# Kernel optimization log

Measured on AMD Instinct MI355X. Metric: run time of the kernel, lower is better.

The kernel has to match this reference:

```python
import jax, jax.numpy as jnp
import numpy as np
from jax import lax

N, T, IN, H, HEADS, OUT, E = 20000, 32, 32, 64, 4, 1, 320000


def setup_inputs() -> dict:
    key = jax.random.key(0)
    ks = jax.random.split(key, 18)
    s = 0.1
    inp = {
        "x": jax.random.normal(ks[0], (N, T, IN), jnp.float32),
        "edge_index": jax.random.randint(ks[1], (2, E), 0, N, dtype=jnp.int32),
        # LSTM layer 0 (PyTorch gate order i,f,g,o)
        "l0_Wih": jax.random.normal(ks[2], (4 * H, IN), jnp.float32) * s,
        "l0_Whh": jax.random.normal(ks[3], (4 * H, H), jnp.float32) * s,
        "l0_bih": jax.random.normal(ks[4], (4 * H,), jnp.float32) * s,
        "l0_bhh": jax.random.normal(ks[5], (4 * H,), jnp.float32) * s,
        # LSTM layer 1
        "l1_Wih": jax.random.normal(ks[6], (4 * H, H), jnp.float32) * s,
        "l1_Whh": jax.random.normal(ks[7], (4 * H, H), jnp.float32) * s,
        "l1_bih": jax.random.normal(ks[8], (4 * H,), jnp.float32) * s,
        "l1_bhh": jax.random.normal(ks[9], (4 * H,), jnp.float32) * s,
        # GAT layer 1: in=H, out=H, heads=HEADS (concat)
        "g1_w": jax.random.normal(ks[10], (H, HEADS * H), jnp.float32) * s,
        "g1_as": jax.random.normal(ks[11], (1, HEADS, H), jnp.float32) * s,
        "g1_ad": jax.random.normal(ks[12], (1, HEADS, H), jnp.float32) * s,
        "g1_b": jnp.zeros((HEADS * H,), jnp.float32),
        # GAT layer 2: in=HEADS*H, out=OUT, heads=1
        "g2_w": jax.random.normal(ks[13], (HEADS * H, OUT), jnp.float32) * s,
        "g2_as": jax.random.normal(ks[14], (1, 1, OUT), jnp.float32) * s,
        "g2_ad": jax.random.normal(ks[15], (1, 1, OUT), jnp.float32) * s,
        "g2_b": jnp.zeros((OUT,), jnp.float32),
    }
    return inp


def _lstm_layer(x, Wih, Whh, bih, bhh):
    # x: [N, T, F] -> [N, T, H]
    n = x.shape[0]
    h0 = jnp.zeros((n, Whh.shape[1]), x.dtype)

    def step(carry, xt):
        h, c = carry
        g = xt @ Wih.T + h @ Whh.T + bih + bhh  # [N, 4H]
        i, f, gg, o = jnp.split(g, 4, axis=-1)
        c = jax.nn.sigmoid(f) * c + jax.nn.sigmoid(i) * jnp.tanh(gg)
        h = jax.nn.sigmoid(o) * jnp.tanh(c)
        return (h, c), h

    _, hs = lax.scan(step, (h0, h0), jnp.swapaxes(x, 0, 1))
    return jnp.swapaxes(hs, 0, 1)


def _gat(x, src, dst, n, W, a_src, a_dst, b, heads, outc):
    # PyG GATConv (eval mode, add_self_loops already applied to src/dst)
    xh = (x @ W).reshape(n, heads, outc)              # [N, heads, C]
    al_s = (xh * a_src).sum(-1)                       # [N, heads]
    al_d = (xh * a_dst).sum(-1)
    e = jax.nn.leaky_relu(al_s[src] + al_d[dst], 0.2)  # [E, heads]
    m = jax.ops.segment_max(e, dst, num_segments=n)
    m = jnp.where(jnp.isfinite(m), m, 0.0)
    ex = jnp.exp(e - m[dst])
    den = jax.ops.segment_sum(ex, dst, num_segments=n)
    w = ex / (den[dst] + 1e-16)                       # segment softmax over dst
    out = jax.ops.segment_sum(xh[src] * w[..., None], dst, num_segments=n)
    return out.reshape(n, heads * outc) + b


def reference(x, edge_index, l0_Wih, l0_Whh, l0_bih, l0_bhh, l1_Wih, l1_Whh,
              l1_bih, l1_bhh, g1_w, g1_as, g1_ad, g1_b, g2_w, g2_as, g2_ad, g2_b):
    n = x.shape[0]
    loops = jnp.arange(n, dtype=edge_index.dtype)
    ei = jnp.concatenate([edge_index, jnp.stack([loops, loops])], axis=1)
    src, dst = ei[0], ei[1]
    h = _lstm_layer(x, l0_Wih, l0_Whh, l0_bih, l0_bhh)
    h = _lstm_layer(h, l1_Wih, l1_Whh, l1_bih, l1_bhh)
    h = h[:, -1, :]  # node features from last timestep
    h = jax.nn.relu(_gat(h, src, dst, n, g1_w, g1_as, g1_ad, g1_b, HEADS, H))
    return _gat(h, src, dst, n, g2_w, g2_as, g2_ad, g2_b, 1, OUT)
```

## Files before the change

### kernel.cpp

```cpp
#include <hip/hip_runtime.h>
#include <math.h>

#define NN   20000
#define TT   32
#define INF_ 32
#define HID  64
#define NH   4
#define EE   320000
#define ETOT (EE + NN)
#define ZROW 168
#define NB   80

typedef __attribute__((ext_vector_type(8))) short bf16x8;
typedef __attribute__((ext_vector_type(4))) float f32x4;

static __device__ __forceinline__ float lrelu(float x){ return x>0.0f ? x : 0.2f*x; }

static __device__ __forceinline__ unsigned short f2bf(float f){
  unsigned u = __float_as_uint(f);
  unsigned r = u + 0x7fffu + ((u>>16)&1u);
  return (unsigned short)(r>>16);
}
static __device__ __forceinline__ float bf2f(unsigned short h){ return __uint_as_float(((unsigned)h)<<16); }

static __device__ __forceinline__ int zpos(int kq){
  return (kq&3) + (((kq>>4)&1)<<2) + (((kq>>2)&3)<<3);
}

static __device__ __forceinline__ float lstm_cell(float gi, float gf, float gg, float go, float& c){
  float ef = __expf(-gf), ei = __expf(-gi), eg = __expf(-2.0f*gg);
  float pN = c*(1.0f+ei)*(1.0f+eg) + (1.0f-eg)*(1.0f+ef);
  float pD = (1.0f+ef)*(1.0f+ei)*(1.0f+eg);
  float cc = pN * __builtin_amdgcn_rcpf(pD);
  c = cc;
  float eo = __expf(-go), ec = __expf(-2.0f*cc);
  return (1.0f-ec) * __builtin_amdgcn_rcpf((1.0f+eo)*(1.0f+ec));
}

static __device__ __forceinline__ void edge_sd(const int* __restrict__ ei, int e, int& s, int& d){
  if (e < EE){ s = ei[e]; d = ei[EE + e]; } else { s = e - EE; d = s; }
}

__global__ void kzero_int(int* __restrict__ p, int n){
  int i = blockIdx.x*256 + threadIdx.x;
  if (i < n) p[i] = 0;
}

__global__ void pack_weights(const float* __restrict__ Wih0, const float* __restrict__ Whh0,
                             const float* __restrict__ bih0, const float* __restrict__ bhh0,
                             const float* __restrict__ Wih1, const float* __restrict__ Whh1,
                             const float* __restrict__ bih1, const float* __restrict__ bhh1,
                             unsigned short* __restrict__ Wpk,
                             float* __restrict__ b0, float* __restrict__ b1){
  int idx = blockIdx.x*256 + threadIdx.x;
  if (idx < 49152){
    int fb = idx >> 9;
    int h  = fb & 1;
    int t2 = fb >> 1;
    int ks = t2 % 3, tl = t2 / 3;
    int r  = idx & 511;
    int l  = r >> 3, j = r & 7;
    int pr = l & 15;
    int g  = (pr&3)*64 + tl*4 + (pr>>2);
    int k  = ks*32 + 4*(l>>4) + (j & 3) + 16*(j >> 2);
    float src = (k < 32) ? Wih0[g*32 + k] : Whh0[g*64 + (k - 32)];
    unsigned short hi = f2bf(src);
    Wpk[idx] = h ? f2bf(src - bf2f(hi)) : hi;
  } else if (idx < 114688){
    int idx2 = idx - 49152;
    int fb = idx2 >> 9;
    int h  = fb & 1;
    int t2 = fb >> 1;
    int ks = t2 & 3, tl = t2 >> 2;
    int r  = idx2 & 511;
    int l  = r >> 3, j = r & 7;
    int pr = l & 15;
    int g  = (pr&3)*64 + tl*4 + (pr>>2);
    int k  = ks*32 + 4*(l>>4) + (j & 3) + 16*(j >> 2);
    float src = (k < 64) ? Wih1[g*64 + k] : Whh1[g*64 + (k - 64)];
    unsigned short hi = f2bf(src);
    Wpk[idx] = h ? f2bf(src - bf2f(hi)) : hi;
  } else {
    int m = idx - 114688;
    if (m < 256) b0[m] = bih0[m] + bhh0[m];
    else if (m < 512) b1[m-256] = bih1[m-256] + bhh1[m-256];
  }
}

__global__ void count_deg(const int* __restrict__ ei, int* __restrict__ deg){
  int e = blockIdx.x*256 + threadIdx.x;
  if (e >= ETOT) return;
  int s, d; edge_sd(ei, e, s, d);
  atomicAdd(deg + d, 1);
}

__global__ void scan_deg(const int* __restrict__ deg, int* __restrict__ indptr, int* __restrict__ cursor){
  __shared__ int part[256];
  const int t = threadIdx.x;
  const int CH = (NN + 255) / 256;
  const int c0 = t * CH;
  int sum = 0;
  for (int i=0;i<CH;i++){ int idx=c0+i; if (idx<NN) sum += deg[idx]; }
  part[t] = sum; __syncthreads();
  int val = sum;
  for (int off=1; off<256; off<<=1){
    int add = (t>=off) ? part[t-off] : 0;
    __syncthreads();
    val += add; part[t] = val;
    __syncthreads();
  }
  int run = val - sum;
  for (int i=0;i<CH;i++){
    int idx=c0+i;
    if (idx<NN){ indptr[idx]=run; cursor[idx]=run; run += deg[idx]; }
  }
  if (t == 0) indptr[NN] = ETOT;
}

__global__ void scatter_edges(const int* __restrict__ ei, int* __restrict__ cursor, int* __restrict__ csr_src){
  int e = blockIdx.x*256 + threadIdx.x;
  if (e >= ETOT) return;
  int s, d; edge_sd(ei, e, s, d);
  int pos = atomicAdd(cursor + d, 1);
  csr_src[pos] = s;
}

#define PIN_LOAD(dst, p) asm volatile( \
    "global_load_dwordx4 %0, %1, off\n\t" \
    "s_waitcnt vmcnt(0)" \
    : "=&v"(dst) : "v"(p))

__global__ __launch_bounds__(1024)
__attribute__((amdgpu_waves_per_eu(4, 4)))
void lstm_mfma(
    const float* __restrict__ x,
    const unsigned short* __restrict__ Wpk,
    const float* __restrict__ b0, const float* __restrict__ b1,
    float* __restrict__ h1out)
{
  __shared__ unsigned short Zh[NB*ZROW];
  __shared__ unsigned short Zl[NB*ZROW];

  const int tid  = threadIdx.x;
  const int lane = tid & 63;
  const int w    = __builtin_amdgcn_readfirstlane(tid >> 6);
  const int ln15 = lane & 15;
  const int lq   = lane >> 4;
  const int gbase = blockIdx.x * NB;

  const bf16x8* wp = (const bf16x8*)Wpk;

  bf16x8 wA0h[3], wA0l[3], wA1h[4], wA1l[4];
#pragma unroll
  for (int ks=0; ks<3; ++ks){
    PIN_LOAD(wA0h[ks], wp + ((w*3+ks)*2+0)*64 + lane);
    PIN_LOAD(wA0l[ks], wp + ((w*3+ks)*2+1)*64 + lane);
  }
#pragma unroll
  for (int ks=0; ks<4; ++ks){
    PIN_LOAD(wA1h[ks], wp + 6144 + ((w*4+ks)*2+0)*64 + lane);
    PIN_LOAD(wA1l[ks], wp + 6144 + ((w*4+ks)*2+1)*64 + lane);
  }

  f32x4 bv0, bv1;
  {
    const int u = w*4 + lq;
#pragma unroll
    for (int j=0; j<4; ++j){ bv0[j] = b0[j*64+u]; bv1[j] = b1[j*64+u]; }
  }

  const int hs_ = lq + ((w & 4) ? 4 : 0) + 8*(w & 3);
  const int uc0 = (1 + (w>>3))*32 + hs_;
  const int uc1 = (3 + (w>>3))*32 + hs_;

  const int xn = tid >> 3;
  const int xk = (tid & 7) * 4;
  const int xslot = (((xk>>2)&3)<<3) + (((xk>>4)&1)<<2);
  const float* xp = x + (size_t)(gbase + ((xn < NB) ? xn : 0))*(TT*INF_) + xk;
  const bool xth = (tid < 640);

#define XSTAGE(v) {                                                       \
    unsigned pkA, pkB, plA, plB;                                          \
    asm("v_cvt_pk_bf16_f32 %0,%1,%2":"=v"(pkA):"v"((v).x),"v"((v).y));    \
    asm("v_cvt_pk_bf16_f32 %0,%1,%2":"=v"(pkB):"v"((v).z),"v"((v).w));    \
    float l0_ = (v).x - __uint_as_float(pkA<<16);                         \
    float l1_ = (v).y - __uint_as_float(pkA & 0xffff0000u);               \
    float l2_ = (v).z - __uint_as_float(pkB<<16);                         \
    float l3_ = (v).w - __uint_as_float(pkB & 0xffff0000u);               \
    asm("v_cvt_pk_bf16_f32 %0,%1,%2":"=v"(plA):"v"(l0_),"v"(l1_));        \
    asm("v_cvt_pk_bf16_f32 %0,%1,%2":"=v"(plB):"v"(l2_),"v"(l3_));        \
    *(uint2*)&Zh[xn*ZROW + xslot] = make_uint2(pkA, pkB);                 \
    *(uint2*)&Zl[xn*ZROW + xslot] = make_uint2(plA, plB); }

  for (int i = tid; i < NB*ZROW/2; i += 1024){ ((unsigned*)Zh)[i] = 0; ((unsigned*)Zl)[i] = 0; }
  __syncthreads();
  if (xth){
    float4 v = *(const float4*)xp;
    XSTAGE(v);
  }
  __syncthreads();

  float c0[5], c1[5];
#pragma unroll
  for (int i=0;i<5;i++){ c0[i]=0.f; c1[i]=0.f; }
  f32x4 aL1[5];

#define ZFRAG(Zb, node, ck) (*(const bf16x8*)&Zb[(node)*ZROW + (ck)*32 + lq*8])

#define MF(acc, A, B) acc = __builtin_amdgcn_mfma_f32_16x16x32_bf16((A),(B),(acc),0,0,0)

#define WPAIR(ha, hb, GA, GB, col) {                                      \
    unsigned pk_, pl_;                                                    \
    asm("v_cvt_pk_bf16_f32 %0,%1,%2":"=v"(pk_):"v"(ha),"v"(hb));          \
    float la_ = (ha) - __uint_as_float(pk_<<16);                          \
    float lb_ = (hb) - __uint_as_float(pk_ & 0xffff0000u);                \
    asm("v_cvt_pk_bf16_f32 %0,%1,%2":"=v"(pl_):"v"(la_),"v"(lb_));        \
    Zh[((GA)*16+ln15)*ZROW + (col)] = (unsigned short)pk_;                \
    Zh[((GB)*16+ln15)*ZROW + (col)] = (unsigned short)(pk_>>16);          \
    Zl[((GA)*16+ln15)*ZROW + (col)] = (unsigned short)pl_;                \
    Zl[((GB)*16+ln15)*ZROW + (col)] = (unsigned short)(pl_>>16); }

#define WSINGLE(hv, GG, col) {                                            \
    const int _n = (GG)*16 + ln15;                                        \
    const unsigned short _hh = f2bf(hv);                                  \
    Zh[_n*ZROW + (col)] = _hh;                                            \
    Zl[_n*ZROW + (col)] = f2bf((hv) - bf2f(_hh)); }

#define CHUNK(ACCS, CK, WH, WL)                                           \
    _Pragma("unroll")                                                     \
    for (int GG=0; GG<5; ++GG){                                           \
      const bf16x8 zh = ZFRAG(Zh, GG*16+ln15, CK);                        \
      const bf16x8 zl = ZFRAG(Zl, GG*16+ln15, CK);                        \
      MF(ACCS[GG], WH, zh); MF(ACCS[GG], WH, zl); MF(ACCS[GG], WL, zh);   \
    }

  for (int t=0; t<TT; ++t){
    float4 xv;
    const bool dox = xth && (t+1 < TT);
    if (dox) xv = *(const float4*)(xp + (size_t)(t+1)*INF_);

    f32x4 aL0[5];
#pragma unroll
    for (int GG=0; GG<5; ++GG) aL0[GG] = bv0;

    CHUNK(aL0, 0, wA0h[0], wA0l[0]);

    if (t > 0){
      float h0_ = lstm_cell(aL1[0][0], aL1[0][1], aL1[0][2], aL1[0][3], c1[0]);
      float h1_ = lstm_cell(aL1[1][0], aL1[1][1], aL1[1][2], aL1[1][3], c1[1]);
      float h2_ = lstm_cell(aL1[2][0], aL1[2][1], aL1[2][2], aL1[2][3], c1[2]);
      float h3_ = lstm_cell(aL1[3][0], aL1[3][1], aL1[3][2], aL1[3][3], c1[3]);
      float h4_ = lstm_cell(aL1[4][0], aL1[4][1], aL1[4][2], aL1[4][3], c1[4]);
      WPAIR(h0_, h1_, 0, 1, uc1); WPAIR(h2_, h3_, 2, 3, uc1); WSINGLE(h4_, 4, uc1);
    }

    CHUNK(aL0, 1, wA0h[1], wA0l[1]);
    CHUNK(aL0, 2, wA0h[2], wA0l[2]);
    __syncthreads();

#pragma unroll
    for (int GG=0; GG<5; ++GG) aL1[GG] = bv1;

    CHUNK(aL1, 3, wA1h[2], wA1l[2]);

    {
      float h0_ = lstm_cell(aL0[0][0], aL0[0][1], aL0[0][2], aL0[0][3], c0[0]);
      float h1_ = lstm_cell(aL0[1][0], aL0[1][1], aL0[1][2], aL0[1][3], c0[1]);
      float h2_ = lstm_cell(aL0[2][0], aL0[2][1], aL0[2][2], aL0[2][3], c0[2]);
      float h3_ = lstm_cell(aL0[3][0], aL0[3][1], aL0[3][2], aL0[3][3], c0[3]);
      float h4_ = lstm_cell(aL0[4][0], aL0[4][1], aL0[4][2], aL0[4][3], c0[4]);
      WPAIR(h0_, h1_, 0, 1, uc0); WPAIR(h2_, h3_, 2, 3, uc0); WSINGLE(h4_, 4, uc0);
    }
    if (dox) XSTAGE(xv);

    CHUNK(aL1, 4, wA1h[3], wA1l[3]);
    __syncthreads();

    CHUNK(aL1, 1, wA1h[0], wA1l[0]);
    CHUNK(aL1, 2, wA1h[1], wA1l[1]);
  }

  {
    float h0_ = lstm_cell(aL1[0][0], aL1[0][1], aL1[0][2], aL1[0][3], c1[0]);
    float h1_ = lstm_cell(aL1[1][0], aL1[1][1], aL1[1][2], aL1[1][3], c1[1]);
    float h2_ = lstm_cell(aL1[2][0], aL1[2][1], aL1[2][2], aL1[2][3], c1[2]);
    float h3_ = lstm_cell(aL1[3][0], aL1[3][1], aL1[3][2], aL1[3][3], c1[3]);
    float h4_ = lstm_cell(aL1[4][0], aL1[4][1], aL1[4][2], aL1[4][3], c1[4]);
    WPAIR(h0_, h1_, 0, 1, uc1); WPAIR(h2_, h3_, 2, 3, uc1); WSINGLE(h4_, 4, uc1);
  }
  __syncthreads();

  for (int o = tid; o < NB*64; o += 1024){
    const int n = o >> 6, u = o & 63;
    const int zp = (3 + (u>>5))*32 + zpos(u & 31);
    h1out[(size_t)(gbase+n)*64 + u] = bf2f(Zh[n*ZROW + zp]) + bf2f(Zl[n*ZROW + zp]);
  }
#undef ZFRAG
#undef MF
#undef WPAIR
#undef WSINGLE
#undef CHUNK
#undef XSTAGE
}

__global__ __launch_bounds__(256) void gat1_prep(const float* __restrict__ h1, const float* __restrict__ W,
  const float* __restrict__ as_, const float* __restrict__ ad_,
  float* __restrict__ xh, float* __restrict__ als, float* __restrict__ ald)
{
  __shared__ float hs[16][64];
  const int nb0 = blockIdx.x * 16;
  const int o  = threadIdx.x;
  const int q  = o >> 6, u = o & 63;
  for (int i = o; i < 1024; i += 256){
    hs[i>>6][i&63] = h1[(size_t)(nb0 + (i>>6))*64 + (i&63)];
  }
  __syncthreads();
  float acc[16];
#pragma unroll
  for (int nd=0; nd<16; ++nd) acc[nd] = 0.f;
  for (int k=0; k<64; ++k){
    const float wv = W[k*256 + o];
#pragma unroll
    for (int nd=0; nd<16; ++nd) acc[nd] = fmaf(hs[nd][k], wv, acc[nd]);
  }
  const float asv = as_[o], adv = ad_[o];
#pragma unroll
  for (int nd=0; nd<16; ++nd){
    xh[(size_t)(nb0+nd)*256 + o] = acc[nd];
    float ps = acc[nd] * asv;
    float pd = acc[nd] * adv;
#pragma unroll
    for (int off=32; off>=1; off>>=1){ ps += __shfl_xor(ps, off); pd += __shfl_xor(pd, off); }
    if (u == 0){ als[(nb0+nd)*4 + q] = ps; ald[(nb0+nd)*4 + q] = pd; }
  }
}

__global__ __launch_bounds__(256) void gat1_gather(
  const int* __restrict__ indptr, const int* __restrict__ csr_src,
  const float* __restrict__ als, const float* __restrict__ ald,
  const float* __restrict__ xh,  const float* __restrict__ b1g,
  const float* __restrict__ w2,  const float* __restrict__ as2, const float* __restrict__ ad2,
  float* __restrict__ xh2, float* __restrict__ a2s, float* __restrict__ a2d)
{
  const int d = blockIdx.x*4 + (threadIdx.x >> 6);
  const int lane = threadIdx.x & 63;
  if (d >= NN) return;
  const int p0 = indptr[d], p1 = indptr[d+1];

  float aldv[4];
#pragma unroll
  for (int q=0;q<4;q++) aldv[q] = ald[d*4+q];

  float mx[4];
#pragma unroll
  for (int q=0;q<4;q++) mx[q] = -3.4e38f;
  for (int e=p0+lane; e<p1; e+=64){
    int s = csr_src[e];
#pragma unroll
    for (int q=0;q<4;q++){
      float ev = lrelu(als[s*4+q] + aldv[q]);
      mx[q] = fmaxf(mx[q], ev);
    }
  }
#pragma unroll
  for (int off=32; off>=1; off>>=1){
#pragma unroll
    for (int q=0;q<4;q++) mx[q] = fmaxf(mx[q], __shfl_xor(mx[q], off));
  }

  const int q = lane >> 4;
  const float mq = mx[q];
  const float aldq = aldv[q];
  float ax=0.f, ay=0.f, az=0.f, aw=0.f, den=0.f;
  int s_next = (p0 < p1) ? csr_src[p0] : 0;
  for (int e=p0; e<p1; ++e){
    const int s = s_next;
    if (e+1 < p1) s_next = csr_src[e+1];
    float ev = lrelu(als[s*4+q] + aldq);
    float ex = __expf(ev - mq);
    den += ex;
    float4 v = *(const float4*)(xh + (size_t)s*256 + lane*4);
    ax = fmaf(ex, v.x, ax); ay = fmaf(ex, v.y, ay);
    az = fmaf(ex, v.z, az); aw = fmaf(ex, v.w, aw);
  }
  const float rr = 1.0f/(den + 1e-16f);
  const int o = lane*4;
  float v0 = ax*rr + b1g[o+0];
  float v1 = ay*rr + b1g[o+1];
  float v2 = az*rr + b1g[o+2];
  float v3 = aw*rr + b1g[o+3];
  v0 = v0>0.f?v0:0.f; v1 = v1>0.f?v1:0.f; v2 = v2>0.f?v2:0.f; v3 = v3>0.f?v3:0.f;
  float part = v0*w2[o+0] + v1*w2[o+1] + v2*w2[o+2] + v3*w2[o+3];
#pragma unroll
  for (int off=32; off>=1; off>>=1) part += __shfl_xor(part, off);
  if (lane == 0){
    xh2[d] = part;
    a2s[d] = part * as2[0];
    a2d[d] = part * ad2[0];
  }
}

__global__ __launch_bounds__(256) void gat2_gather(
  const int* __restrict__ indptr, const int* __restrict__ csr_src,
  const float* __restrict__ a2s, const float* __restrict__ a2d,
  const float* __restrict__ xh2, const float* __restrict__ b2,
  float* __restrict__ out)
{
  const int d = blockIdx.x*4 + (threadIdx.x >> 6);
  const int lane = threadIdx.x & 63;
  if (d >= NN) return;
  const int p0 = indptr[d], p1 = indptr[d+1];
  const float add = a2d[d];

  float mx = -3.4e38f;
  for (int e=p0+lane; e<p1; e+=64){
    int s = csr_src[e];
    mx = fmaxf(mx, lrelu(a2s[s] + add));
  }
#pragma unroll
  for (int off=32; off>=1; off>>=1) mx = fmaxf(mx, __shfl_xor(mx, off));

  float den = 0.f, num = 0.f;
  for (int e=p0+lane; e<p1; e+=64){
    int s = csr_src[e];
    float ev = lrelu(a2s[s] + add);
    float ex = __expf(ev - mx);
    den += ex;
    num = fmaf(ex, xh2[s], num);
  }
#pragma unroll
  for (int off=32; off>=1; off>>=1){ den += __shfl_xor(den, off); num += __shfl_xor(num, off); }
  if (lane == 0) out[d] = num/(den + 1e-16f) + b2[0];
}

extern "C" void kernel_launch(void* const* d_in, const int* in_sizes, int n_in,
                              void* d_out, int out_size, void* d_ws, size_t ws_size,
                              hipStream_t stream)
{
  const float* x    = (const float*)d_in[0];
  const int*   ei   = (const int*)d_in[1];
  const float* Wih0 = (const float*)d_in[2];
  const float* Whh0 = (const float*)d_in[3];
  const float* bih0 = (const float*)d_in[4];
  const float* bhh0 = (const float*)d_in[5];
  const float* Wih1 = (const float*)d_in[6];
  const float* Whh1 = (const float*)d_in[7];
  const float* bih1 = (const float*)d_in[8];
  const float* bhh1 = (const float*)d_in[9];
  const float* g1w  = (const float*)d_in[10];
  const float* g1as = (const float*)d_in[11];
  const float* g1ad = (const float*)d_in[12];
  const float* g1b  = (const float*)d_in[13];
  const float* g2w  = (const float*)d_in[14];
  const float* g2as = (const float*)d_in[15];
  const float* g2ad = (const float*)d_in[16];
  const float* g2b  = (const float*)d_in[17];

  float* ws  = (float*)d_ws;
  unsigned short* Wpk = (unsigned short*)ws;
  float* b0  = ws + 57344;
  float* b1  = b0 + 256;
  float* h1  = b1 + 256;
  float* xh  = h1 + 1280000;
  float* als = xh + 5120000;
  float* ald = als + 80000;
  float* xh2 = ald + 80000;
  float* a2s = xh2 + 20000;
  float* a2d = a2s + 20000;
  int*   deg    = (int*)(a2d + 20000);
  int*   indptr = deg + 20000;
  int*   cursor = indptr + 20001;
  int*   csr    = cursor + 20000;

  kzero_int<<<(NN+255)/256, 256, 0, stream>>>(deg, NN);
  pack_weights<<<450, 256, 0, stream>>>(Wih0,Whh0,bih0,bhh0,Wih1,Whh1,bih1,bhh1,Wpk,b0,b1);
  count_deg<<<(ETOT+255)/256, 256, 0, stream>>>(ei, deg);
  scan_deg<<<1, 256, 0, stream>>>(deg, indptr, cursor);
  scatter_edges<<<(ETOT+255)/256, 256, 0, stream>>>(ei, cursor, csr);
  lstm_mfma<<<250, 1024, 0, stream>>>(x, Wpk, b0, b1, h1);
  gat1_prep<<<NN/16, 256, 0, stream>>>(h1, g1w, g1as, g1ad, xh, als, ald);
  gat1_gather<<<(NN+3)/4, 256, 0, stream>>>(indptr, csr, als, ald, xh, g1b, g2w, g2as, g2ad, xh2, a2s, a2d);
  gat2_gather<<<(NN+3)/4, 256, 0, stream>>>(indptr, csr, a2s, a2d, xh2, g2b, (float*)d_out);
}
```

Measured before the change: 405.2 us.

## Interleave LSTM hi/lo bf16 tiles, parallelize degree scan, enlarge GAT prep tile

The LSTM shared-memory state goes from two separate hi/lo bf16 arrays to one interleaved array, so the hi and lo fragments for a node sit next to each other with a different row stride. This changes the LDS bank access pattern for the MFMA operand reads and the h writes. The single-block degree scan becomes a three-kernel multi-block scan, trading one serial kernel for more launches. gat1_prep now processes 32 nodes per block instead of 16, which raises register use per thread in exchange for more reuse of each weight load.

New measurement: 355.2 us. -12.3%, faster.

```diff
diff --git a/kernel.cpp b/kernel.cpp
--- a/kernel.cpp
+++ b/kernel.cpp
@@ -8,8 +8,9 @@
 #define NH   4
 #define EE   320000
 #define ETOT (EE + NN)
-#define ZROW 168
+#define ZRW  328
 #define NB   80
+#define SCB  80
 
 typedef __attribute__((ext_vector_type(8))) short bf16x8;
 typedef __attribute__((ext_vector_type(4))) float f32x4;
@@ -94,27 +95,38 @@
   atomicAdd(deg + d, 1);
 }
 
-__global__ void scan_deg(const int* __restrict__ deg, int* __restrict__ indptr, int* __restrict__ cursor){
-  __shared__ int part[256];
-  const int t = threadIdx.x;
-  const int CH = (NN + 255) / 256;
-  const int c0 = t * CH;
-  int sum = 0;
-  for (int i=0;i<CH;i++){ int idx=c0+i; if (idx<NN) sum += deg[idx]; }
-  part[t] = sum; __syncthreads();
-  int val = sum;
+__global__ void scan_part(const int* __restrict__ deg, int* __restrict__ part){
+  __shared__ int s[256];
+  const int b = blockIdx.x, t = threadIdx.x;
+  int v = (t < 250) ? deg[b*250 + t] : 0;
+  s[t] = v; __syncthreads();
+  for (int off=128; off>=1; off>>=1){ if (t<off) s[t]+=s[t+off]; __syncthreads(); }
+  if (t==0) part[b] = s[0];
+}
+
+__global__ void scan_tops(int* __restrict__ part){
+  if (threadIdx.x==0){
+    int run=0;
+    for (int i=0;i<SCB;i++){ int v=part[i]; part[i]=run; run+=v; }
+  }
+}
+
+__global__ void scan_fill(const int* __restrict__ deg, const int* __restrict__ part,
+                          int* __restrict__ indptr, int* __restrict__ cursor){
+  __shared__ int s[256];
+  const int b = blockIdx.x, t = threadIdx.x;
+  int v = (t < 250) ? deg[b*250 + t] : 0;
+  s[t] = v; __syncthreads();
+  int val = v;
   for (int off=1; off<256; off<<=1){
-    int add = (t>=off) ? part[t-off] : 0;
+    int add = (t>=off) ? s[t-off] : 0;
     __syncthreads();
-    val += add; part[t] = val;
+    val += add; s[t] = val;
     __syncthreads();
   }
-  int run = val - sum;
-  for (int i=0;i<CH;i++){
-    int idx=c0+i;
-    if (idx<NN){ indptr[idx]=run; cursor[idx]=run; run += deg[idx]; }
-  }
-  if (t == 0) indptr[NN] = ETOT;
+  int excl = val - v + part[b];
+  if (t < 250){ indptr[b*250 + t] = excl; cursor[b*250 + t] = excl; }
+  if (b == SCB-1 && t == 0) indptr[NN] = ETOT;
 }
 
 __global__ void scatter_edges(const int* __restrict__ ei, int* __restrict__ cursor, int* __restrict__ csr_src){
@@ -138,8 +150,7 @@
     const float* __restrict__ b0, const float* __restrict__ b1,
     float* __restrict__ h1out)
 {
-  __shared__ unsigned short Zh[NB*ZROW];
-  __shared__ unsigned short Zl[NB*ZROW];
+  __shared__ unsigned short Zc[NB*ZRW];
 
   const int tid  = threadIdx.x;
   const int lane = tid & 63;
@@ -169,13 +180,14 @@
     for (int j=0; j<4; ++j){ bv0[j] = b0[j*64+u]; bv1[j] = b1[j*64+u]; }
   }
 
-  const int hs_ = lq + ((w & 4) ? 4 : 0) + 8*(w & 3);
-  const int uc0 = (1 + (w>>3))*32 + hs_;
-  const int uc1 = (3 + (w>>3))*32 + hs_;
+  const int colbase = ((w&3)<<4) + lq + (((w>>2)&1)<<2);
+  const int uc0 = (1 + (w>>3))*64 + colbase;
+  const int uc1 = (3 + (w>>3))*64 + colbase;
 
   const int xn = tid >> 3;
   const int xk = (tid & 7) * 4;
-  const int xslot = (((xk>>2)&3)<<3) + (((xk>>4)&1)<<2);
+  const int p0 = (((xk>>4)&1)<<2) + (((xk>>2)&3)<<3);
+  const int xoff = ((p0>>3)<<4) + (p0&7);
   const float* xp = x + (size_t)(gbase + ((xn < NB) ? xn : 0))*(TT*INF_) + xk;
   const bool xth = (tid < 640);
 
@@ -189,10 +201,10 @@
     float l3_ = (v).w - __uint_as_float(pkB & 0xffff0000u);               \
     asm("v_cvt_pk_bf16_f32 %0,%1,%2":"=v"(plA):"v"(l0_),"v"(l1_));        \
     asm("v_cvt_pk_bf16_f32 %0,%1,%2":"=v"(plB):"v"(l2_),"v"(l3_));        \
-    *(uint2*)&Zh[xn*ZROW + xslot] = make_uint2(pkA, pkB);                 \
-    *(uint2*)&Zl[xn*ZROW + xslot] = make_uint2(plA, plB); }
-
-  for (int i = tid; i < NB*ZROW/2; i += 1024){ ((unsigned*)Zh)[i] = 0; ((unsigned*)Zl)[i] = 0; }
+    *(uint2*)&Zc[xn*ZRW + xoff]     = make_uint2(pkA, pkB);               \
+    *(uint2*)&Zc[xn*ZRW + xoff + 8] = make_uint2(plA, plB); }
+
+  for (int i = tid; i < NB*ZRW/2; i += 1024) ((unsigned*)Zc)[i] = 0;
   __syncthreads();
   if (xth){
     float4 v = *(const float4*)xp;
@@ -205,32 +217,31 @@
   for (int i=0;i<5;i++){ c0[i]=0.f; c1[i]=0.f; }
   f32x4 aL1[5];
 
-#define ZFRAG(Zb, node, ck) (*(const bf16x8*)&Zb[(node)*ZROW + (ck)*32 + lq*8])
-
 #define MF(acc, A, B) acc = __builtin_amdgcn_mfma_f32_16x16x32_bf16((A),(B),(acc),0,0,0)
 
-#define WPAIR(ha, hb, GA, GB, col) {                                      \
+#define WPAIR(ha, hb, GA, GB, colh) {                                     \
     unsigned pk_, pl_;                                                    \
     asm("v_cvt_pk_bf16_f32 %0,%1,%2":"=v"(pk_):"v"(ha),"v"(hb));          \
     float la_ = (ha) - __uint_as_float(pk_<<16);                          \
     float lb_ = (hb) - __uint_as_float(pk_ & 0xffff0000u);                \
     asm("v_cvt_pk_bf16_f32 %0,%1,%2":"=v"(pl_):"v"(la_),"v"(lb_));        \
-    Zh[((GA)*16+ln15)*ZROW + (col)] = (unsigned short)pk_;                \
-    Zh[((GB)*16+ln15)*ZROW + (col)] = (unsigned short)(pk_>>16);          \
-    Zl[((GA)*16+ln15)*ZROW + (col)] = (unsigned short)pl_;                \
-    Zl[((GB)*16+ln15)*ZROW + (col)] = (unsigned short)(pl_>>16); }
-
-#define WSINGLE(hv, GG, col) {                                            \
+    Zc[((GA)*16+ln15)*ZRW + (colh)]     = (unsigned short)pk_;            \
+    Zc[((GB)*16+ln15)*ZRW + (colh)]     = (unsigned short)(pk_>>16);      \
+    Zc[((GA)*16+ln15)*ZRW + (colh) + 8] = (unsigned short)pl_;            \
+    Zc[((GB)*16+ln15)*ZRW + (colh) + 8] = (unsigned short)(pl_>>16); }
+
+#define WSINGLE(hv, GG, colh) {                                           \
     const int _n = (GG)*16 + ln15;                                        \
     const unsigned short _hh = f2bf(hv);                                  \
-    Zh[_n*ZROW + (col)] = _hh;                                            \
-    Zl[_n*ZROW + (col)] = f2bf((hv) - bf2f(_hh)); }
+    Zc[_n*ZRW + (colh)]     = _hh;                                        \
+    Zc[_n*ZRW + (colh) + 8] = f2bf((hv) - bf2f(_hh)); }
 
 #define CHUNK(ACCS, CK, WH, WL)                                           \
     _Pragma("unroll")                                                     \
     for (int GG=0; GG<5; ++GG){                                           \
-      const bf16x8 zh = ZFRAG(Zh, GG*16+ln15, CK);                        \
-      const bf16x8 zl = ZFRAG(Zl, GG*16+ln15, CK);                        \
+      const int nd_ = GG*16 + ln15;                                       \
+      const bf16x8 zh = *(const bf16x8*)&Zc[nd_*ZRW + (CK)*64 + lq*16];   \
+      const bf16x8 zl = *(const bf16x8*)&Zc[nd_*ZRW + (CK)*64 + lq*16+8]; \
       MF(ACCS[GG], WH, zh); MF(ACCS[GG], WH, zl); MF(ACCS[GG], WL, zh);   \
     }
 
@@ -292,10 +303,10 @@
 
   for (int o = tid; o < NB*64; o += 1024){
     const int n = o >> 6, u = o & 63;
-    const int zp = (3 + (u>>5))*32 + zpos(u & 31);
-    h1out[(size_t)(gbase+n)*64 + u] = bf2f(Zh[n*ZROW + zp]) + bf2f(Zl[n*ZROW + zp]);
-  }
-#undef ZFRAG
+    const int p = zpos(u & 31);
+    const int ch = (3 + (u>>5))*64 + ((p>>3)<<4) + (p&7);
+    h1out[(size_t)(gbase+n)*64 + u] = bf2f(Zc[n*ZRW + ch]) + bf2f(Zc[n*ZRW + ch + 8]);
+  }
 #undef MF
 #undef WPAIR
 #undef WSINGLE
@@ -307,25 +318,25 @@
   const float* __restrict__ as_, const float* __restrict__ ad_,
   float* __restrict__ xh, float* __restrict__ als, float* __restrict__ ald)
 {
-  __shared__ float hs[16][64];
-  const int nb0 = blockIdx.x * 16;
+  __shared__ float hs[32][64];
+  const int nb0 = blockIdx.x * 32;
   const int o  = threadIdx.x;
   const int q  = o >> 6, u = o & 63;
-  for (int i = o; i < 1024; i += 256){
+  for (int i = o; i < 2048; i += 256){
     hs[i>>6][i&63] = h1[(size_t)(nb0 + (i>>6))*64 + (i&63)];
   }
   __syncthreads();
-  float acc[16];
-#pragma unroll
-  for (int nd=0; nd<16; ++nd) acc[nd] = 0.f;
+  float acc[32];
+#pragma unroll
+  for (int nd=0; nd<32; ++nd) acc[nd] = 0.f;
   for (int k=0; k<64; ++k){
     const float wv = W[k*256 + o];
 #pragma unroll
-    for (int nd=0; nd<16; ++nd) acc[nd] = fmaf(hs[nd][k], wv, acc[nd]);
+    for (int nd=0; nd<32; ++nd) acc[nd] = fmaf(hs[nd][k], wv, acc[nd]);
   }
   const float asv = as_[o], adv = ad_[o];
 #pragma unroll
-  for (int nd=0; nd<16; ++nd){
+  for (int nd=0; nd<32; ++nd){
     xh[(size_t)(nb0+nd)*256 + o] = acc[nd];
     float ps = acc[nd] * asv;
     float pd = acc[nd] * adv;
@@ -471,14 +482,17 @@
   int*   indptr = deg + 20000;
   int*   cursor = indptr + 20001;
   int*   csr    = cursor + 20000;
+  int*   spart  = csr + 340000;
 
   kzero_int<<<(NN+255)/256, 256, 0, stream>>>(deg, NN);
   pack_weights<<<450, 256, 0, stream>>>(Wih0,Whh0,bih0,bhh0,Wih1,Whh1,bih1,bhh1,Wpk,b0,b1);
   count_deg<<<(ETOT+255)/256, 256, 0, stream>>>(ei, deg);
-  scan_deg<<<1, 256, 0, stream>>>(deg, indptr, cursor);
+  scan_part<<<SCB, 256, 0, stream>>>(deg, spart);
+  scan_tops<<<1, 64, 0, stream>>>(spart);
+  scan_fill<<<SCB, 256, 0, stream>>>(deg, spart, indptr, cursor);
   scatter_edges<<<(ETOT+255)/256, 256, 0, stream>>>(ei, cursor, csr);
   lstm_mfma<<<250, 1024, 0, stream>>>(x, Wpk, b0, b1, h1);
-  gat1_prep<<<NN/16, 256, 0, stream>>>(h1, g1w, g1as, g1ad, xh, als, ald);
+  gat1_prep<<<NN/32, 256, 0, stream>>>(h1, g1w, g1as, g1ad, xh, als, ald);
   gat1_gather<<<(NN+3)/4, 256, 0, stream>>>(indptr, csr, als, ald, xh, g1b, g2w, g2as, g2ad, xh2, a2s, a2d);
   gat2_gather<<<(NN+3)/4, 256, 0, stream>>>(indptr, csr, a2s, a2d, xh2, g2b, (float*)d_out);
 }
```
